# Kernel optimization log

Measured on AMD Instinct MI355X. Metric: run time of the kernel, lower is better.

The kernel has to match this reference:

```python
import jax, jax.numpy as jnp
import numpy as np

EMBED_DIM = 1024
NUM_HEADS = 16
HEAD_DIM = EMBED_DIM // NUM_HEADS


def setup_inputs() -> dict:
    key = jax.random.key(0)
    k_x, k_wqkv, k_bqkv, k_wo, k_bo = jax.random.split(key, 5)
    B, T, C = 4, 2048, EMBED_DIM
    bound = 1.0 / np.sqrt(C)
    return {
        "x": jax.random.normal(k_x, (B, T, C), dtype=jnp.float32),
        "w_qkv": jax.random.uniform(k_wqkv, (C, 3 * C), jnp.float32, -bound, bound),
        "b_qkv": jax.random.uniform(k_bqkv, (3 * C,), jnp.float32, -bound, bound),
        "w_out": jax.random.uniform(k_wo, (C, C), jnp.float32, -bound, bound),
        "b_out": jax.random.uniform(k_bo, (C,), jnp.float32, -bound, bound),
    }


def reference(x, w_qkv, b_qkv, w_out, b_out):
    B, T, C = x.shape
    H, D = NUM_HEADS, HEAD_DIM
    qkv = x @ w_qkv + b_qkv                       # [B,T,3C]
    qkv = qkv.reshape(B, T, 3, H, D)
    q, k, v = qkv[:, :, 0], qkv[:, :, 1], qkv[:, :, 2]  # [B,T,H,D]
    scale = 1.0 / np.sqrt(D).astype(np.float32)
    scores = jnp.einsum("bqhd,bkhd->bhqk", q, k) * scale  # [B,H,T,T]
    causal = jnp.tril(jnp.ones((T, T), dtype=bool))
    scores = jnp.where(causal, scores, -jnp.inf)
    attn = jax.nn.softmax(scores, axis=-1)
    # dropout p=0.0 / eval mode -> identity
    ctx = jnp.einsum("bhqk,bkhd->bqhd", attn, v).reshape(B, T, C)
    return ctx @ w_out + b_out
```

## Files before the change

### kernel.cpp

```cpp
#include <hip/hip_runtime.h>
#include <hip/hip_bf16.h>

#define NB 4
#define NT 2048
#define NC 1024
#define NH 16
#define ND 64
#define BT (NB*NT)
#define LOG2E 1.4426950408889634f
#define NEG_BIG (-3.0e38f)
#define MLC 28.853900817779268f

typedef __attribute__((ext_vector_type(8))) short bf16x8;
typedef __attribute__((ext_vector_type(4))) float f32x4;

static __device__ __forceinline__ short f2bf(float f) {
    union { float f; unsigned u; } v; v.f = f;
    unsigned r = (v.u + 0x7fffu + ((v.u >> 16) & 1u)) >> 16;
    return (short)r;
}

static __device__ __forceinline__ unsigned pk2(float a, float b) {
#if __has_builtin(__builtin_amdgcn_cvt_pk_bf16_f32)
    auto v = __builtin_amdgcn_cvt_pk_bf16_f32(a, b);
    union { decltype(v) v; unsigned u; } c; c.v = v; return c.u;
#else
    return (unsigned)(unsigned short)f2bf(a) | ((unsigned)(unsigned short)f2bf(b) << 16);
#endif
}

static __device__ __forceinline__ f32x4 mfma16(bf16x8 a, bf16x8 b, f32x4 c) {
    return __builtin_amdgcn_mfma_f32_16x16x32_bf16(a, b, c, 0, 0, 0);
}

static __device__ __forceinline__ float fexp2(float x) {
#if __has_builtin(__builtin_amdgcn_exp2f)
    return __builtin_amdgcn_exp2f(x);
#else
    return exp2f(x);
#endif
}

template<int GOFF>
static __device__ __forceinline__ void gload_lds16(const short* g, short* l) {
    __builtin_amdgcn_global_load_lds(
        (const __attribute__((address_space(1))) void*)g,
        (__attribute__((address_space(3))) void*)l,
        16, GOFF, 0);
}

__global__ __launch_bounds__(256)
void xcvt(const float* __restrict__ x, short* __restrict__ xb)
{
    const size_t i = ((size_t)blockIdx.x * 256 + threadIdx.x) * 8;
    float4 f0 = *(const float4*)(x + i);
    float4 f1 = *(const float4*)(x + i + 4);
    uint4 p;
    p.x = pk2(f0.x, f0.y); p.y = pk2(f0.z, f0.w);
    p.z = pk2(f1.x, f1.y); p.w = pk2(f1.z, f1.w);
    *(uint4*)(xb + i) = p;
}

__global__ __launch_bounds__(256)
void transpose_w(const float* __restrict__ w, short* __restrict__ wt, int R, int Cn)
{
    __shared__ short t[64][72];
    const int tid = threadIdx.x;
    const int r0 = blockIdx.x * 64;
    const int c0 = blockIdx.y * 64;
    {
        const int rl = tid >> 2, c4 = (tid & 3) << 4;
        const float* src = w + (size_t)(r0 + rl) * Cn + c0 + c4;
        float4 f0 = *(const float4*)(src + 0);
        float4 f1 = *(const float4*)(src + 4);
        float4 f2 = *(const float4*)(src + 8);
        float4 f3 = *(const float4*)(src + 12);
        short* d = &t[rl][c4];
        d[0]=f2bf(f0.x); d[1]=f2bf(f0.y); d[2]=f2bf(f0.z); d[3]=f2bf(f0.w);
        d[4]=f2bf(f1.x); d[5]=f2bf(f1.y); d[6]=f2bf(f1.z); d[7]=f2bf(f1.w);
        d[8]=f2bf(f2.x); d[9]=f2bf(f2.y); d[10]=f2bf(f2.z); d[11]=f2bf(f2.w);
        d[12]=f2bf(f3.x); d[13]=f2bf(f3.y); d[14]=f2bf(f3.z); d[15]=f2bf(f3.w);
    }
    __syncthreads();
    {
        const int cl = tid >> 2, r4 = (tid & 3) << 4;
        bf16x8 p0, p1;
#pragma unroll
        for (int j = 0; j < 8; ++j) { p0[j] = t[r4 + j][cl]; p1[j] = t[r4 + 8 + j][cl]; }
        short* dst = wt + (size_t)(c0 + cl) * R + r0 + r4;
        *(bf16x8*)dst       = p0;
        *(bf16x8*)(dst + 8) = p1;
    }
}

__global__ __launch_bounds__(512, 2)
void qkv_gemm8(const short* __restrict__ xb, const short* __restrict__ wt,
               const float* __restrict__ bias,
               short* __restrict__ q, short* __restrict__ k, short* __restrict__ vt)
{
    __shared__ short aLds[2][256 * 64];
    __shared__ short bLds[2][256 * 64];
    const int tid  = threadIdx.x;
    const int lane = tid & 63;
    const int wave = tid >> 6;
    const int waveM = wave & 1;
    const int waveN = wave >> 1;
    const int quad = lane >> 4;
    const int l15  = lane & 15;
    const int l7   = l15 & 7;
    const int m0 = blockIdx.x * 256;
    const int n0 = blockIdx.y * 256;

    const int rsub = lane >> 3;
    const int gcol = ((lane & 7) ^ rsub) * 8;

    f32x4 acc[8][4];
#pragma unroll
    for (int i = 0; i < 8; ++i)
#pragma unroll
        for (int j = 0; j < 4; ++j) acc[i][j] = 0.0f;

    bf16x8 aF[4][2];
    bf16x8 bF[2][2][2];

    auto stA = [&](int p, int kt, int h) {
#pragma unroll
        for (int i = 0; i < 2; ++i) {
            const int rb = h*128 + i*64 + wave*8;
            gload_lds16<0>(xb + (size_t)(m0 + rb + rsub) * NC + kt*64 + gcol,
                           &aLds[p][rb * 64]);
        }
    };
    auto stB = [&](int p, int kt, int h) {
#pragma unroll
        for (int i = 0; i < 2; ++i) {
            const int rb = h*128 + i*64 + wave*8;
            gload_lds16<0>(wt + (size_t)(n0 + rb + rsub) * NC + kt*64 + gcol,
                           &bLds[p][rb * 64]);
        }
    };
    auto rdA = [&](int p, int mh) {
#pragma unroll
        for (int mi = 0; mi < 4; ++mi)
#pragma unroll
            for (int kd = 0; kd < 2; ++kd) {
                const int r = waveM*128 + mh*64 + mi*16 + l15;
                aF[mi][kd] = *(const bf16x8*)
                    &aLds[p][r*64 + (((kd*4 + quad) ^ l7) * 8)];
            }
    };
    auto rdB = [&](int p, int nh) {
#pragma unroll
        for (int ni = 0; ni < 2; ++ni)
#pragma unroll
            for (int kd = 0; kd < 2; ++kd) {
                const int r = waveN*64 + nh*32 + ni*16 + l15;
                bF[nh][ni][kd] = *(const bf16x8*)
                    &bLds[p][r*64 + (((kd*4 + quad) ^ l7) * 8)];
            }
    };
    auto mmQ = [&](int mh, int nh) {
        __builtin_amdgcn_s_setprio(1);
#pragma unroll
        for (int mi = 0; mi < 4; ++mi)
#pragma unroll
            for (int ni = 0; ni < 2; ++ni) {
                f32x4 c = acc[mh*4 + mi][nh*2 + ni];
                c = mfma16(aF[mi][0], bF[nh][ni][0], c);
                c = mfma16(aF[mi][1], bF[nh][ni][1], c);
                acc[mh*4 + mi][nh*2 + ni] = c;
            }
        __builtin_amdgcn_s_setprio(0);
    };

    stB(0, 0, 0); stB(0, 0, 1);
    stA(0, 0, 0); stA(0, 0, 1);
    stB(1, 1, 0); stB(1, 1, 1);
    asm volatile("s_waitcnt vmcnt(4)" ::: "memory");
    __builtin_amdgcn_s_barrier();

#pragma unroll 1
    for (int kt = 0; kt < 16; ++kt) {
        const int p = kt & 1;
        rdA(p, 0); rdB(p, 0);
        if (kt + 1 < 16) stA(p ^ 1, kt + 1, 0);
        asm volatile("s_waitcnt lgkmcnt(8)" ::: "memory");
        __builtin_amdgcn_s_barrier();
        asm volatile("s_waitcnt lgkmcnt(0)" ::: "memory");
        mmQ(0, 0);
        __builtin_amdgcn_s_barrier();
        rdB(p, 1);
        if (kt + 1 < 16) stA(p ^ 1, kt + 1, 1);
        __builtin_amdgcn_s_barrier();
        asm volatile("s_waitcnt lgkmcnt(0)" ::: "memory");
        mmQ(0, 1);
        __builtin_amdgcn_s_barrier();
        rdA(p, 1);
        if (kt + 2 < 16) stB(p, kt + 2, 0);
        __builtin_amdgcn_s_barrier();
        asm volatile("s_waitcnt lgkmcnt(0)" ::: "memory");
        mmQ(1, 1);
        __builtin_amdgcn_s_barrier();
        if (kt + 2 < 16) stB(p, kt + 2, 1);
        __builtin_amdgcn_s_barrier();
        mmQ(1, 0);
        if (kt + 2 < 16)      asm volatile("s_waitcnt vmcnt(4)" ::: "memory");
        else if (kt + 1 < 16) asm volatile("s_waitcnt vmcnt(0)" ::: "memory");
        __builtin_amdgcn_s_barrier();
    }

#pragma unroll
    for (int mi = 0; mi < 8; ++mi) {
#pragma unroll
        for (int ni = 0; ni < 4; ++ni) {
            const int n = n0 + waveN*64 + ni*16 + l15;
            const float bb = bias[n];
            const int s = n >> 10;
            const int h = (n >> 6) & 15;
            const int d = n & 63;
#pragma unroll
            for (int r = 0; r < 4; ++r) {
                const int m = m0 + waveM*128 + mi*16 + quad*4 + r;
                const int b = m >> 11;
                const int t = m & (NT - 1);
                const float val = acc[mi][ni][r] + bb;
                const size_t bhx = (size_t)(b * NH + h);
                if (s == 0)      q [(bhx * NT + t) * ND + d] = f2bf(val * 0.125f);
                else if (s == 1) k [(bhx * NT + t) * ND + d] = f2bf(val);
                else             vt[(bhx * ND + d) * NT + t] = f2bf(val);
            }
        }
    }
}

__global__ __launch_bounds__(256)
void attn(const short* __restrict__ q, const short* __restrict__ k,
          const short* __restrict__ vt, short* __restrict__ ctx)
{
    __shared__ short kbuf[2][64 * 64];
    __shared__ short vbuf[2][64 * 64];
    __shared__ short pbuf[4][32 * 64];
    const int tid  = threadIdx.x;
    const int lane = tid & 63;
    const int wave = tid >> 6;
    const int quad = lane >> 4;
    const int l15  = lane & 15;
    const int l7   = l15 & 7;
    const int bh = blockIdx.x;
    const int b  = bh >> 4;
    const int h  = bh & 15;

    const short* Qp = q  + (size_t)bh * NT * ND;
    const short* Kp = k  + (size_t)bh * NT * ND;
    const short* Vp = vt + (size_t)bh * ND * NT;

    const int srow   = lane >> 3;
    const int schunk = ((lane & 7) ^ srow) * 8;
    short* pw = &pbuf[wave][0];

    for (int half = 0; half < 2; ++half) {
        const int qblock = half ? (15 - (int)blockIdx.y) : (int)blockIdx.y;
        const int qb  = qblock * 128;
        const int wq0 = qb + wave * 32;
        const int ktB = 2 * qblock + 2;

        bf16x8 qf[2][2];
#pragma unroll
        for (int mi = 0; mi < 2; ++mi)
#pragma unroll
            for (int kd = 0; kd < 2; ++kd)
                qf[mi][kd] = *(const bf16x8*)(Qp + (size_t)(wq0 + mi*16 + l15) * ND + kd*32 + quad*8);

        f32x4 ot[4][2];
        f32x4 lv[2];
#pragma unroll
        for (int di = 0; di < 4; ++di)
#pragma unroll
            for (int mi = 0; mi < 2; ++mi) ot[di][mi] = 0.0f;
        lv[0] = 0.0f; lv[1] = 0.0f;

        {
            const short* Ks = Kp + (size_t)(wave*16 + srow) * ND + schunk;
            gload_lds16<0>(Ks,          &kbuf[0][(wave*16    ) * 64]);
            gload_lds16<0>(Ks + 8*ND,   &kbuf[0][(wave*16 + 8) * 64]);
            const short* Vs = Vp + (size_t)(wave*16 + srow) * NT + schunk;
            gload_lds16<0>(Vs,          &vbuf[0][(wave*16    ) * 64]);
            gload_lds16<0>(Vs + 8*NT,   &vbuf[0][(wave*16 + 8) * 64]);
        }

        for (int kt = 0; kt < ktB; ++kt) {
            const int p  = kt & 1;
            const int kb = kt << 6;
            __syncthreads();

            if (kt + 1 < ktB) {
                const int kb2 = kb + 64;
                const short* Ks = Kp + (size_t)(kb2 + wave*16 + srow) * ND + schunk;
                gload_lds16<0>(Ks,        &kbuf[1-p][(wave*16    ) * 64]);
                gload_lds16<0>(Ks + 8*ND, &kbuf[1-p][(wave*16 + 8) * 64]);
                const short* Vs = Vp + (size_t)(wave*16 + srow) * NT + kb2 + schunk;
                gload_lds16<0>(Vs,        &vbuf[1-p][(wave*16    ) * 64]);
                gload_lds16<0>(Vs + 8*NT, &vbuf[1-p][(wave*16 + 8) * 64]);
            }

            if (kb > wq0 + 31) continue;

            bf16x8 kf[4][2];
#pragma unroll
            for (int ni = 0; ni < 4; ++ni)
#pragma unroll
                for (int kd = 0; kd < 2; ++kd)
                    kf[ni][kd] = *(const bf16x8*)
                        &kbuf[p][(ni*16 + l15)*64 + (((kd*4 + quad) ^ l7) * 8)];

            f32x4 st[4][2];
#pragma unroll
            for (int ni = 0; ni < 4; ++ni)
#pragma unroll
                for (int mi = 0; mi < 2; ++mi) {
                    st[ni][mi] = 0.0f;
                    st[ni][mi] = mfma16(kf[ni][0], qf[mi][0], st[ni][mi]);
                    st[ni][mi] = mfma16(kf[ni][1], qf[mi][1], st[ni][mi]);
                }

            if (kb + 63 > wq0) {
#pragma unroll
                for (int ni = 0; ni < 4; ++ni)
#pragma unroll
                    for (int mi = 0; mi < 2; ++mi) {
                        const int qrow = wq0 + mi*16 + l15;
#pragma unroll
                        for (int r = 0; r < 4; ++r) {
                            const int key = kb + ni*16 + quad*4 + r;
                            if (key > qrow) st[ni][mi][r] = NEG_BIG;
                        }
                    }
            }

#pragma unroll
            for (int mi = 0; mi < 2; ++mi) {
#pragma unroll
                for (int ni = 0; ni < 4; ++ni) {
#pragma unroll
                    for (int r = 0; r < 4; ++r)
                        st[ni][mi][r] = fexp2(fmaf(st[ni][mi][r], LOG2E, -MLC));
                    lv[mi] += st[ni][mi];
                    const f32x4 v = st[ni][mi];
                    *(uint2*)&pw[(mi*16 + l15)*64
                                 + (((2*ni + (quad >> 1)) ^ l7) * 8)
                                 + (quad & 1) * 4] =
                        make_uint2(pk2(v[0], v[1]), pk2(v[2], v[3]));
                }
            }

            bf16x8 vf[4][2], pf[2][2];
#pragma unroll
            for (int di = 0; di < 4; ++di)
#pragma unroll
                for (int kd = 0; kd < 2; ++kd)
                    vf[di][kd] = *(const bf16x8*)
                        &vbuf[p][(di*16 + l15)*64 + (((kd*4 + quad) ^ l7) * 8)];
#pragma unroll
            for (int mi = 0; mi < 2; ++mi)
#pragma unroll
                for (int kd = 0; kd < 2; ++kd)
                    pf[mi][kd] = *(const bf16x8*)
                        &pw[(mi*16 + l15)*64 + (((kd*4 + quad) ^ l7) * 8)];

#pragma unroll
            for (int di = 0; di < 4; ++di)
#pragma unroll
                for (int mi = 0; mi < 2; ++mi) {
                    ot[di][mi] = mfma16(vf[di][0], pf[mi][0], ot[di][mi]);
                    ot[di][mi] = mfma16(vf[di][1], pf[mi][1], ot[di][mi]);
                }
        }

#pragma unroll
        for (int mi = 0; mi < 2; ++mi) {
            float l = lv[mi][0] + lv[mi][1] + lv[mi][2] + lv[mi][3];
            l += __shfl_xor(l, 16);
            l += __shfl_xor(l, 32);
            const float inv = 1.0f / l;
            const int t = wq0 + mi*16 + l15;
            short* dst = ctx + ((size_t)(b * NT + t)) * NC + h*64 + quad*4;
#pragma unroll
            for (int di = 0; di < 4; ++di) {
                const f32x4 v = ot[di][mi] * inv;
                *(uint2*)(dst + di*16) = make_uint2(pk2(v[0], v[1]), pk2(v[2], v[3]));
            }
        }
        __syncthreads();
    }
}

__global__ __launch_bounds__(256)
void out_gemm(const short* __restrict__ a, const short* __restrict__ wt,
              const float* __restrict__ bias, float* __restrict__ out)
{
    __shared__ short aLds[128 * 64];
    __shared__ short bLds[128 * 64];
    const int tid  = threadIdx.x;
    const int lane = tid & 63;
    const int wave = tid >> 6;
    const int waveM = wave & 1;
    const int waveN = wave >> 1;
    const int quad = lane >> 4;
    const int l15  = lane & 15;
    const int l7   = l15 & 7;
    const int m0 = blockIdx.x * 128;
    const int n0 = blockIdx.y * 128;

    const int rsub   = lane >> 3;
    const int cchunk = (lane & 7) ^ rsub;
    const int gcol   = cchunk * 8;

    f32x4 acc[4][4];
#pragma unroll
    for (int i = 0; i < 4; ++i)
#pragma unroll
        for (int j = 0; j < 4; ++j) acc[i][j] = 0.0f;

    for (int k0 = 0; k0 < NC; k0 += 64) {
#pragma unroll
        for (int i = 0; i < 4; ++i) {
            const int rbase = wave * 32 + i * 8;
            gload_lds16<0>(a + (size_t)(m0 + rbase + rsub) * NC + k0 + gcol,
                           &aLds[rbase * 64]);
        }
#pragma unroll
        for (int i = 0; i < 4; ++i) {
            const int rbase = wave * 32 + i * 8;
            gload_lds16<0>(wt + (size_t)(n0 + rbase + rsub) * NC + k0 + gcol,
                           &bLds[rbase * 64]);
        }
        __syncthreads();

#pragma unroll
        for (int kd = 0; kd < 2; ++kd) {
            bf16x8 af[4], bfr[4];
#pragma unroll
            for (int mi = 0; mi < 4; ++mi) {
                const int r = waveM*64 + mi*16 + l15;
                af[mi] = *(const bf16x8*)&aLds[r*64 + (((kd*4 + quad) ^ l7) * 8)];
            }
#pragma unroll
            for (int ni = 0; ni < 4; ++ni) {
                const int r = waveN*64 + ni*16 + l15;
                bfr[ni] = *(const bf16x8*)&bLds[r*64 + (((kd*4 + quad) ^ l7) * 8)];
            }
#pragma unroll
            for (int mi = 0; mi < 4; ++mi)
#pragma unroll
                for (int ni = 0; ni < 4; ++ni)
                    acc[mi][ni] = mfma16(af[mi], bfr[ni], acc[mi][ni]);
        }
        __syncthreads();
    }

#pragma unroll
    for (int mi = 0; mi < 4; ++mi) {
#pragma unroll
        for (int ni = 0; ni < 4; ++ni) {
            const int n = n0 + waveN*64 + ni*16 + l15;
            const float bb = bias[n];
#pragma unroll
            for (int r = 0; r < 4; ++r) {
                const int m = m0 + waveM*64 + mi*16 + quad*4 + r;
                out[(size_t)m * NC + n] = acc[mi][ni][r] + bb;
            }
        }
    }
}

extern "C" void kernel_launch(void* const* d_in, const int* in_sizes, int n_in,
                              void* d_out, int out_size, void* d_ws, size_t ws_size,
                              hipStream_t stream)
{
    const float* x     = (const float*)d_in[0];
    const float* w_qkv = (const float*)d_in[1];
    const float* b_qkv = (const float*)d_in[2];
    const float* w_out = (const float*)d_in[3];
    const float* b_out = (const float*)d_in[4];
    float* out = (float*)d_out;

    const size_t SZ = (size_t)NB * NH * NT * ND;
    short* q   = (short*)d_ws;
    short* kk  = q  + SZ;
    short* vt  = kk + SZ;
    short* ctx = vt + SZ;
    short* xbf = ctx + SZ;
    short* wTq = ctx;
    short* wTo = xbf;

    hipLaunchKernelGGL(xcvt, dim3(BT*NC/(256*8)), dim3(256), 0, stream, x, xbf);
    hipLaunchKernelGGL(transpose_w, dim3(16, 48), dim3(256), 0, stream,
                       w_qkv, wTq, NC, 3*NC);
    hipLaunchKernelGGL(qkv_gemm8, dim3(BT/256, (3*NC)/256), dim3(512), 0, stream,
                       xbf, wTq, b_qkv, q, kk, vt);
    hipLaunchKernelGGL(attn, dim3(NB*NH, 8), dim3(256), 0, stream,
                       q, kk, vt, ctx);
    hipLaunchKernelGGL(transpose_w, dim3(16, 16), dim3(256), 0, stream,
                       w_out, wTo, NC, NC);
    hipLaunchKernelGGL(out_gemm, dim3(BT/128, NC/128), dim3(256), 0, stream,
                       ctx, wTo, b_out, out);
}
```

Baseline: 285.4 us.

## Shrink QKV GEMM N-tile to 128 and use triple-buffered LDS pipeline

After: 273.4 us. 4.2% less time.

```diff
diff --git a/kernel.cpp b/kernel.cpp
--- a/kernel.cpp
+++ b/kernel.cpp
@@ -98,8 +98,8 @@
                const float* __restrict__ bias,
                short* __restrict__ q, short* __restrict__ k, short* __restrict__ vt)
 {
-    __shared__ short aLds[2][256 * 64];
-    __shared__ short bLds[2][256 * 64];
+    __shared__ short aLds[3][256 * 64];
+    __shared__ short bLds[3][128 * 64];
     const int tid  = threadIdx.x;
     const int lane = tid & 63;
     const int wave = tid >> 6;
@@ -109,111 +109,102 @@
     const int l15  = lane & 15;
     const int l7   = l15 & 7;
     const int m0 = blockIdx.x * 256;
-    const int n0 = blockIdx.y * 256;
+    const int n0 = blockIdx.y * 128;
 
     const int rsub = lane >> 3;
     const int gcol = ((lane & 7) ^ rsub) * 8;
 
-    f32x4 acc[8][4];
+    f32x4 acc[8][2];
 #pragma unroll
     for (int i = 0; i < 8; ++i)
 #pragma unroll
-        for (int j = 0; j < 4; ++j) acc[i][j] = 0.0f;
+        for (int j = 0; j < 2; ++j) acc[i][j] = 0.0f;
 
     bf16x8 aF[4][2];
-    bf16x8 bF[2][2][2];
-
-    auto stA = [&](int p, int kt, int h) {
-#pragma unroll
-        for (int i = 0; i < 2; ++i) {
-            const int rb = h*128 + i*64 + wave*8;
+    bf16x8 bF[2][2];
+
+    auto stA = [&](int bufi, int kt) {
+#pragma unroll
+        for (int c = 0; c < 4; ++c) {
+            const int rb = c*64 + wave*8;
             gload_lds16<0>(xb + (size_t)(m0 + rb + rsub) * NC + kt*64 + gcol,
-                           &aLds[p][rb * 64]);
+                           &aLds[bufi][rb * 64]);
         }
     };
-    auto stB = [&](int p, int kt, int h) {
-#pragma unroll
-        for (int i = 0; i < 2; ++i) {
-            const int rb = h*128 + i*64 + wave*8;
+    auto stB = [&](int bufi, int kt) {
+#pragma unroll
+        for (int c = 0; c < 2; ++c) {
+            const int rb = c*64 + wave*8;
             gload_lds16<0>(wt + (size_t)(n0 + rb + rsub) * NC + kt*64 + gcol,
-                           &bLds[p][rb * 64]);
+                           &bLds[bufi][rb * 64]);
         }
     };
-    auto rdA = [&](int p, int mh) {
+    auto rdA = [&](int bufi, int mh) {
 #pragma unroll
         for (int mi = 0; mi < 4; ++mi)
 #pragma unroll
             for (int kd = 0; kd < 2; ++kd) {
                 const int r = waveM*128 + mh*64 + mi*16 + l15;
                 aF[mi][kd] = *(const bf16x8*)
-                    &aLds[p][r*64 + (((kd*4 + quad) ^ l7) * 8)];
+                    &aLds[bufi][r*64 + (((kd*4 + quad) ^ l7) * 8)];
             }
     };
-    auto rdB = [&](int p, int nh) {
+    auto rdB = [&](int bufi) {
 #pragma unroll
         for (int ni = 0; ni < 2; ++ni)
 #pragma unroll
             for (int kd = 0; kd < 2; ++kd) {
-                const int r = waveN*64 + nh*32 + ni*16 + l15;
-                bF[nh][ni][kd] = *(const bf16x8*)
-                    &bLds[p][r*64 + (((kd*4 + quad) ^ l7) * 8)];
+                const int r = waveN*32 + ni*16 + l15;
+                bF[ni][kd] = *(const bf16x8*)
+                    &bLds[bufi][r*64 + (((kd*4 + quad) ^ l7) * 8)];
             }
     };
-    auto mmQ = [&](int mh, int nh) {
+    auto mmQ = [&](int mh) {
         __builtin_amdgcn_s_setprio(1);
 #pragma unroll
         for (int mi = 0; mi < 4; ++mi)
 #pragma unroll
             for (int ni = 0; ni < 2; ++ni) {
-                f32x4 c = acc[mh*4 + mi][nh*2 + ni];
-                c = mfma16(aF[mi][0], bF[nh][ni][0], c);
-                c = mfma16(aF[mi][1], bF[nh][ni][1], c);
-                acc[mh*4 + mi][nh*2 + ni] = c;
+                f32x4 c = acc[mh*4 + mi][ni];
+                c = mfma16(aF[mi][0], bF[ni][0], c);
+                c = mfma16(aF[mi][1], bF[ni][1], c);
+                acc[mh*4 + mi][ni] = c;
             }
         __builtin_amdgcn_s_setprio(0);
     };
 
-    stB(0, 0, 0); stB(0, 0, 1);
-    stA(0, 0, 0); stA(0, 0, 1);
-    stB(1, 1, 0); stB(1, 1, 1);
-    asm volatile("s_waitcnt vmcnt(4)" ::: "memory");
+    stA(0, 0); stB(0, 0);
+    stA(1, 1); stB(1, 1);
+    asm volatile("s_waitcnt vmcnt(6)" ::: "memory");
     __builtin_amdgcn_s_barrier();
 
+    int cur = 0;
 #pragma unroll 1
     for (int kt = 0; kt < 16; ++kt) {
-        const int p = kt & 1;
-        rdA(p, 0); rdB(p, 0);
-        if (kt + 1 < 16) stA(p ^ 1, kt + 1, 0);
+        const int stg = (cur >= 1) ? cur - 1 : 2;
+        rdA(cur, 0); rdB(cur);
+        if (kt + 2 < 16) stA(stg, kt + 2);
         asm volatile("s_waitcnt lgkmcnt(8)" ::: "memory");
         __builtin_amdgcn_s_barrier();
         asm volatile("s_waitcnt lgkmcnt(0)" ::: "memory");
-        mmQ(0, 0);
+        mmQ(0);
         __builtin_amdgcn_s_barrier();
-        rdB(p, 1);
-        if (kt + 1 < 16) stA(p ^ 1, kt + 1, 1);
+        rdA(cur, 1);
+        if (kt + 2 < 16) stB(stg, kt + 2);
         __builtin_amdgcn_s_barrier();
         asm volatile("s_waitcnt lgkmcnt(0)" ::: "memory");
-        mmQ(0, 1);
-        __builtin_amdgcn_s_barrier();
-        rdA(p, 1);
-        if (kt + 2 < 16) stB(p, kt + 2, 0);
-        __builtin_amdgcn_s_barrier();
-        asm volatile("s_waitcnt lgkmcnt(0)" ::: "memory");
-        mmQ(1, 1);
-        __builtin_amdgcn_s_barrier();
-        if (kt + 2 < 16) stB(p, kt + 2, 1);
-        __builtin_amdgcn_s_barrier();
-        mmQ(1, 0);
-        if (kt + 2 < 16)      asm volatile("s_waitcnt vmcnt(4)" ::: "memory");
+        mmQ(1);
+        if (kt + 2 < 16)      asm volatile("s_waitcnt vmcnt(6)" ::: "memory");
         else if (kt + 1 < 16) asm volatile("s_waitcnt vmcnt(0)" ::: "memory");
         __builtin_amdgcn_s_barrier();
+        cur = (cur == 2) ? 0 : cur + 1;
     }
 
 #pragma unroll
     for (int mi = 0; mi < 8; ++mi) {
 #pragma unroll
-        for (int ni = 0; ni < 4; ++ni) {
-            const int n = n0 + waveN*64 + ni*16 + l15;
+        for (int ni = 0; ni < 2; ++ni) {
+            const int n = n0 + waveN*32 + ni*16 + l15;
             const float bb = bias[n];
             const int s = n >> 10;
             const int h = (n >> 6) & 15;
@@ -496,7 +487,7 @@
     hipLaunchKernelGGL(xcvt, dim3(BT*NC/(256*8)), dim3(256), 0, stream, x, xbf);
     hipLaunchKernelGGL(transpose_w, dim3(16, 48), dim3(256), 0, stream,
                        w_qkv, wTq, NC, 3*NC);
-    hipLaunchKernelGGL(qkv_gemm8, dim3(BT/256, (3*NC)/256), dim3(512), 0, stream,
+    hipLaunchKernelGGL(qkv_gemm8, dim3(BT/256, (3*NC)/128), dim3(512), 0, stream,
                        xbf, wTq, b_qkv, q, kk, vt);
     hipLaunchKernelGGL(attn, dim3(NB*NH, 8), dim3(256), 0, stream,
                        q, kk, vt, ctx);
```
